# Optimization experiments

Measured on AMD Instinct MI355X. Metric: run time of the kernel, lower is better.

Reference implementation:

```python
import jax, jax.numpy as jnp
import numpy as np

# Dims (match init_kwargs / input_specs)
B, N, DIM, HEADS, DHEAD, CHUNK = 1, 2048, 1024, 8, 128, 64
HID = 4 * DHEAD            # MemoryMLP expansion_factor=4.0
DI = HEADS * DHEAD         # dim_inner
EPS = 1e-6
MAX_LR = 1.0               # default_step_transform_max_lr


def rmsnorm(x, w):
    return x * jax.lax.rsqrt(jnp.mean(jnp.square(x), -1, keepdims=True) + EPS) * w


def mem_forward(w0, w1, g, x):
    # ResidualNorm(MemoryMLP): y = RMSNorm(gelu(x@w0)@w1)*g + x
    h = jax.nn.gelu(x @ w0, approximate=False) @ w1
    return rmsnorm(h, g) + x


def setup_inputs() -> dict:
    key = jax.random.key(0)
    ks = jax.random.split(key, 12)
    s = lambda i, shape, sc: jax.random.normal(ks[i], shape, jnp.float32) * sc
    return dict(
        x=s(0, (B, N, DIM), 1.0),
        store_norm_w=jnp.ones((DIM,), jnp.float32),
        ret_norm_w=jnp.ones((DIM,), jnp.float32),
        Wq=s(1, (DIM, DI), DIM ** -0.5),
        Wk=s(2, (DIM, DI), DIM ** -0.5),
        Wv=s(3, (DIM, DI), DIM ** -0.5),
        W_step=s(4, (DIM, HEADS), DIM ** -0.5), b_step=jnp.zeros((HEADS,), jnp.float32),
        W_mom=s(5, (DIM, HEADS), DIM ** -0.5), b_mom=jnp.zeros((HEADS,), jnp.float32),
        W_decay=s(6, (DIM, HEADS), DIM ** -0.5), b_decay=jnp.zeros((HEADS,), jnp.float32),
        gate_W=s(7, (DIM, HEADS), DIM ** -0.5),
        combine_W=s(8, (DI, DIM), DI ** -0.5),
        mem_w0=s(9, (HEADS, DHEAD, HID), DHEAD ** -0.5),
        mem_w1=s(10, (HEADS, HID, DHEAD), HID ** -0.5),
        mem_g=jnp.ones((HEADS, DHEAD), jnp.float32),
    )


def reference(x, store_norm_w, ret_norm_w, Wq, Wk, Wv, W_step, b_step,
              W_mom, b_mom, W_decay, b_decay, gate_W, combine_W,
              mem_w0, mem_w1, mem_g):
    b, n, _ = x.shape
    nc = n // CHUNK
    BH = b * HEADS

    # ---- store path ----
    s = rmsnorm(x, store_norm_w)                                 # b n dim
    lr = jax.nn.sigmoid(s @ W_step + b_step) * MAX_LR            # b n h (per-token adaptive step)
    pooled = s.reshape(b, nc, CHUNK, DIM).mean(2)                # b nc dim (AveragePool chunk rep)
    mom = jax.nn.sigmoid(pooled @ W_mom + b_mom)                 # b nc h
    dec = jax.nn.sigmoid(pooled @ W_decay + b_decay)             # b nc h

    def to_chunks(t):  # b n (h d) -> (b h) nc c d
        return t.reshape(b, nc, CHUNK, HEADS, DHEAD).transpose(0, 3, 1, 2, 4).reshape(BH, nc, CHUNK, DHEAD)

    k = to_chunks(s @ Wk)
    v = to_chunks(s @ Wv)
    lr_c = lr.reshape(b, nc, CHUNK, HEADS).transpose(0, 3, 1, 2).reshape(BH, nc, CHUNK)
    mom_bh = mom.transpose(0, 2, 1).reshape(BH, nc)
    dec_bh = dec.transpose(0, 2, 1).reshape(BH, nc)

    # init fast weights per (b h)  (per_head_learned_parameters=True)
    w0 = jnp.broadcast_to(mem_w0[None], (b, HEADS, DHEAD, HID)).reshape(BH, DHEAD, HID)
    w1 = jnp.broadcast_to(mem_w1[None], (b, HEADS, HID, DHEAD)).reshape(BH, HID, DHEAD)
    g = jnp.broadcast_to(mem_g[None], (b, HEADS, DHEAD)).reshape(BH, DHEAD)

    def chunk_loss(w0_, w1_, g_, kc, vc, lrc):
        pred = mem_forward(w0_, w1_, g_, kc)                     # c d
        return jnp.sum(jnp.mean(jnp.square(pred - vc), -1) * lrc)

    grad_chunk = jax.grad(chunk_loss, argnums=(0, 1, 2))
    # vmap over chunks (same weights per chunk, per-sample grads), then over (b h)
    grads = jax.vmap(jax.vmap(grad_chunk, in_axes=(None, None, None, 0, 0, 0)))(w0, w1, g, k, v, lr_c)
    surprises = tuple(-gr for gr in grads)                       # each (BH, nc, ...)

    def combine(a, c):
        ga, xa = a
        gb, xb = c
        return (ga * gb, gb * xa + xb)

    def lin_scan(gates, xs):
        # y_i = gates_i * y_{i-1} + xs_i over chunk axis (axis=1)
        return jax.lax.associative_scan(combine, (gates, xs), axis=1)

    def expand(gates, ref):
        return gates.reshape(gates.shape + (1,) * (ref.ndim - 2))

    # momentum scan per parameter tensor
    updates = tuple(lin_scan(expand(mom_bh, su), su)[1] for su in surprises)

    # weight update scan: W_i = (1 - decay_i) * W_{i-1} + momentum_i, W_{-1} = init
    per_chunk_weights = []
    for upd, w_init in zip(updates, (w0, w1, g)):
        gates = expand(1.0 - dec_bh, upd)
        cumg, y = lin_scan(gates, upd)
        w_seq = y + cumg * w_init[:, None]                       # (BH, nc, ...)
        # retrieval at chunk i uses weights updated through chunk i-1
        per_chunk_weights.append(jnp.concatenate([w_init[:, None], w_seq[:, :-1]], axis=1))
    w0_c, w1_c, g_c = per_chunk_weights

    # ---- retrieve path ----
    r = rmsnorm(x, ret_norm_w)
    q = to_chunks(r @ Wq)                                        # (BH, nc, c, d)
    pred = jax.vmap(jax.vmap(mem_forward))(w0_c, w1_c, g_c, q)   # (BH, nc, c, d)
    out = pred.reshape(b, HEADS, n, DHEAD)                       # b h n d
    gate = jax.nn.sigmoid(r @ gate_W)                            # b n h (retrieve_gate, heads>1)
    out = out * gate.transpose(0, 2, 1)[..., None]
    out = out.transpose(0, 2, 1, 3).reshape(b, n, DI) @ combine_W
    return out
```

## Files before the change

### kernel.cpp

```cpp
#include <hip/hip_runtime.h>
#include <hip/hip_bf16.h>
#include <math.h>

#define NH   8
#define DHD  128
#define HIDN 512
#define CHK  64
#define NCH  32
#define MB   1048576ull

typedef unsigned short u16;
typedef unsigned int   u32;
typedef short s16x8 __attribute__((ext_vector_type(8)));
typedef float f32x4 __attribute__((ext_vector_type(4)));

#define MFMA(a,b,c) __builtin_amdgcn_mfma_f32_16x16x32_bf16((a),(b),(c),0,0,0)

__device__ __forceinline__ float bf2f(u16 v){ return __uint_as_float(((u32)v) << 16); }
__device__ __forceinline__ u16 f2bf(float f){
  u32 u = __float_as_uint(f);
  u += 0x7fffu + ((u >> 16) & 1u);
  return (u16)(u >> 16);
}
__device__ __forceinline__ u32 pack2(float a, float b){
  return (u32)f2bf(a) | ((u32)f2bf(b) << 16);
}
__device__ __forceinline__ float dot2(u32 a, u32 b){
  return __uint_as_float(a << 16)*__uint_as_float(b << 16)
       + __uint_as_float(a & 0xffff0000u)*__uint_as_float(b & 0xffff0000u);
}
__device__ __forceinline__ float waveRedSum(float v){
  #pragma unroll
  for (int off = 32; off; off >>= 1) v += __shfl_xor(v, off);
  return v;
}
__device__ __forceinline__ void gload16(const void* g, void* l){
  __builtin_amdgcn_global_load_lds(
      (const __attribute__((address_space(1))) u32*)g,
      (__attribute__((address_space(3))) u32*)l, 16, 0, 0);
}
__device__ __forceinline__ int swzb(int row, int colb){ return colb ^ ((row & 7) << 4); }
__device__ __forceinline__ int swza(int row, int colb){
  return colb ^ ((row & 7) << 4) ^ (((row >> 3) & 3) << 5);
}


__global__ __launch_bounds__(256) void k_prep(
    const float* __restrict__ Wq, const float* __restrict__ Wk,
    const float* __restrict__ Wv, const float* __restrict__ combW,
    const float* __restrict__ mw0, const float* __restrict__ mw1,
    const float* __restrict__ Wstep, const float* __restrict__ gateW,
    u16* __restrict__ WqT, u16* __restrict__ WkT, u16* __restrict__ WvT, u16* __restrict__ combT,
    u16* __restrict__ w0L, u16* __restrict__ w1L, u16* __restrict__ w1bL, u16* __restrict__ WsgL){
  __shared__ u16 tile[32][34];
  int bid = blockIdx.x, t = threadIdx.x;
  if (bid < 4096){
    int z = bid >> 10, rem = bid & 1023;
    const float* in = (z==0)?Wq:(z==1)?Wk:(z==2)?Wv:combW;
    u16* out = (z==0)?WqT:(z==1)?WkT:(z==2)?WvT:combT;
    int c0 = (rem & 31)*32, r0 = (rem >> 5)*32;
    int tx = t & 31, ty = t >> 5;
    #pragma unroll
    for (int k = 0; k < 4; ++k) tile[ty+k*8][tx] = f2bf(in[(size_t)(r0+ty+k*8)*1024 + c0+tx]);
    __syncthreads();
    #pragma unroll
    for (int k = 0; k < 4; ++k) out[(size_t)(c0+ty+k*8)*1024 + r0+tx] = tile[tx][ty+k*8];
  } else if (bid < 10240){
    int b2 = bid - 4096;
    int which = b2 >> 11;
    int h = (b2 >> 8) & 7;
    int i = (b2 & 255)*256 + t;
    int r = i & 511, blk = i >> 9;
    int lg = r >> 7, lr = (r >> 3) & 15, e = r & 7;
    float v; u16* dst;
    if (which == 0){ int n0 = blk >> 2, ks = blk & 3; int hid = n0*16+lr, d = ks*32+lg*8+e;
      v = mw0[(size_t)h*65536 + (size_t)d*512 + hid]; dst = w0L; }
    else if (which == 1){ int n0 = blk >> 4, ks = blk & 15; int d = n0*16+lr, hid = ks*32+lg*8+e;
      v = mw1[(size_t)h*65536 + (size_t)hid*128 + d]; dst = w1L; }
    else { int n0 = blk >> 2, ks = blk & 3; int hid = n0*16+lr, d = ks*32+lg*8+e;
      v = mw1[(size_t)h*65536 + (size_t)hid*128 + d]; dst = w1bL; }
    dst[(size_t)h*65536 + i] = f2bf(v);
  } else {
    int i = (bid - 10240)*256 + t;
    if (i < 16384){
      int o = i >> 10, k = i & 1023;
      float v = (o < 8) ? Wstep[(size_t)k*8 + o] : gateW[(size_t)k*8 + (o-8)];
      WsgL[i] = f2bf(v);
    }
  }
}

__global__ __launch_bounds__(256) void k_rmsnorm(const float* __restrict__ x,
    const float* __restrict__ wst, const float* __restrict__ wrt,
    u16* __restrict__ s_bf, u16* __restrict__ r_bf){
  int row = blockIdx.x, t = threadIdx.x;
  float4 v = ((const float4*)(x + (size_t)row*1024))[t];
  float ss = v.x*v.x + v.y*v.y + v.z*v.z + v.w*v.w;
  ss = waveRedSum(ss);
  __shared__ float red[4];
  int wv = t >> 6, ln = t & 63;
  if (ln == 0) red[wv] = ss;
  __syncthreads();
  float rr = rsqrtf((red[0]+red[1]+red[2]+red[3])*(1.f/1024.f) + 1e-6f);
  float4 a = ((const float4*)wst)[t];
  float4 b = ((const float4*)wrt)[t];
  uint2 so = make_uint2(pack2(v.x*rr*a.x, v.y*rr*a.y), pack2(v.z*rr*a.z, v.w*rr*a.w));
  uint2 ro = make_uint2(pack2(v.x*rr*b.x, v.y*rr*b.y), pack2(v.z*rr*b.z, v.w*rr*b.w));
  *(uint2*)(s_bf + (size_t)row*1024 + t*4) = so;
  *(uint2*)(r_bf + (size_t)row*1024 + t*4) = ro;
}

__global__ __launch_bounds__(256) void k_lrmd(const u16* __restrict__ s_bf, const u16* __restrict__ r_bf,
    const u16* __restrict__ WsgL, const float* __restrict__ bstep,
    const float* __restrict__ Wmom, const float* __restrict__ bmom,
    const float* __restrict__ Wdec, const float* __restrict__ bdec,
    float* __restrict__ lrc, float* __restrict__ gate,
    float* __restrict__ momb, float* __restrict__ decb){
  int bx = blockIdx.x;
  if (bx < 512){
    int wv = threadIdx.x >> 6, ln = threadIdx.x & 63;
    int tok = bx*4 + wv;
    const u16* sp = s_bf + (size_t)tok*1024 + ln*16;
    const u16* rp = r_bf + (size_t)tok*1024 + ln*16;
    uint4 s0 = *(const uint4*)sp, s1 = *(const uint4*)(sp+8);
    uint4 r0 = *(const uint4*)rp, r1 = *(const uint4*)(rp+8);
    #pragma unroll 4
    for (int o = 0; o < 16; ++o){
      const u16* wp = WsgL + (size_t)o*1024 + ln*16;
      uint4 w0v = *(const uint4*)wp, w1v = *(const uint4*)(wp+8);
      uint4 a0 = (o < 8) ? s0 : r0, a1 = (o < 8) ? s1 : r1;
      float acc = dot2(a0.x,w0v.x)+dot2(a0.y,w0v.y)+dot2(a0.z,w0v.z)+dot2(a0.w,w0v.w)
                + dot2(a1.x,w1v.x)+dot2(a1.y,w1v.y)+dot2(a1.z,w1v.z)+dot2(a1.w,w1v.w);
      acc = waveRedSum(acc);
      if (ln == 0){
        int h = o & 7;
        if (o < 8){
          float v = 1.f/(1.f+expf(-(acc + bstep[h])));
          lrc[((size_t)h*NCH + (tok>>6))*CHK + (tok&63)] = v;
        } else {
          gate[(size_t)tok*8 + h] = 1.f/(1.f+expf(-acc));
        }
      }
    }
  } else {
    __shared__ float plds[1024];
    int c = bx - 512, t = threadIdx.x;
    #pragma unroll
    for (int q = 0; q < 4; ++q){
      int d = q*256 + t;
      float acc = 0.f;
      for (int tt = 0; tt < 64; ++tt) acc += bf2f(s_bf[((size_t)c*64+tt)*1024 + d]);
      plds[d] = acc * (1.f/64.f);
    }
    __syncthreads();
    if (t < 64){
      int ln = t;
      for (int o = 0; o < 16; ++o){
        int h = o & 7;
        const float* W = (o < 8) ? Wmom : Wdec;
        float acc = 0.f;
        for (int k = ln; k < 1024; k += 64) acc += plds[k]*W[(size_t)k*8+h];
        acc = waveRedSum(acc);
        if (ln == 0){
          float bb = (o < 8) ? bmom[h] : bdec[h];
          float v = 1.f/(1.f+expf(-(acc+bb)));
          if (o < 8) momb[h*NCH + c] = v; else decb[h*NCH + c] = v;
        }
      }
    }
  }
}

__device__ __forceinline__ void gemm_body(const u16* __restrict__ A, const u16* __restrict__ BT,
    void* __restrict__ Cp, int mode){
  __shared__ char As[8192];
  __shared__ char Bs[16384];
  int t = threadIdx.x, l = t & 63, w = t >> 6, lr16 = l & 15, lg = l >> 4;
  int wm = w & 1, wn = w >> 1;
  int bm = blockIdx.x*64, bn = blockIdx.y*128;
  f32x4 acc[2][2];
  #pragma unroll
  for (int mt = 0; mt < 2; ++mt)
    #pragma unroll
    for (int nt = 0; nt < 2; ++nt) acc[mt][nt] = (f32x4){0.f,0.f,0.f,0.f};
  for (int k0 = 0; k0 < 1024; k0 += 64){
    gload16(A  + (size_t)(bm + (t>>3))*1024      + k0 + (t&7)*8, As + w*1024);
    gload16(BT + (size_t)(bn + (t>>3))*1024      + k0 + (t&7)*8, Bs + w*1024);
    gload16(BT + (size_t)(bn + 64 + (t>>3))*1024 + k0 + (t&7)*8, Bs + 8192 + w*1024);
    __syncthreads();
    #pragma unroll
    for (int ks = 0; ks < 2; ++ks){
      s16x8 xa[2], yb[2];
      #pragma unroll
      for (int mt = 0; mt < 2; ++mt){ int row = wm*32 + mt*16 + lr16;
        xa[mt] = *(const s16x8*)(As + row*128 + ks*64 + lg*16); }
      #pragma unroll
      for (int nt = 0; nt < 2; ++nt){ int row = wn*32 + nt*16 + lr16;
        yb[nt] = *(const s16x8*)(Bs + row*128 + ks*64 + lg*16); }
      #pragma unroll
      for (int mt = 0; mt < 2; ++mt)
        #pragma unroll
        for (int nt = 0; nt < 2; ++nt) acc[mt][nt] = MFMA(xa[mt], yb[nt], acc[mt][nt]);
    }
    __syncthreads();
  }
  #pragma unroll
  for (int mt = 0; mt < 2; ++mt)
    #pragma unroll
    for (int nt = 0; nt < 2; ++nt)
      #pragma unroll
      for (int j = 0; j < 4; ++j){
        int row = bm + wm*32 + mt*16 + lg*4 + j;
        int coln = bn + wn*32 + nt*16 + lr16;
        if (mode == 0) ((float*)Cp)[(size_t)row*1024 + coln] = acc[mt][nt][j];
        else { int cI = row>>6, tok = row&63, h = coln>>7, d = coln&127;
          ((u16*)Cp)[((size_t)(h*32+cI)*64 + tok)*128 + d] = f2bf(acc[mt][nt][j]); }
      }
}

__global__ __launch_bounds__(512) void k_gemm_bf(const u16* __restrict__ A, const u16* __restrict__ BT,
    void* __restrict__ Cp, int mode){ gemm_body(A, BT, Cp, mode); }

__global__ __launch_bounds__(512) void k_gemm3(
    const u16* __restrict__ s_bf, const u16* __restrict__ r_bf,
    const u16* __restrict__ WkT, const u16* __restrict__ WvT, const u16* __restrict__ WqT,
    u16* __restrict__ Kc, u16* __restrict__ Vc, u16* __restrict__ Qc){
  int z = blockIdx.z;
  const u16* A = (z==2) ? r_bf : s_bf;
  const u16* BT = (z==0) ? WkT : (z==1) ? WvT : WqT;
  u16* C = (z==0) ? Kc : (z==1) ? Vc : Qc;
  gemm_body(A, BT, (void*)C, 1);
}

__global__ __launch_bounds__(512) void k_grad(
    const u16* __restrict__ Kc, const u16* __restrict__ Vc, const float* __restrict__ lrc,
    const u16* __restrict__ w0L, const u16* __restrict__ w1L, const u16* __restrict__ w1bL,
    const float* __restrict__ mg,
    u16* __restrict__ SW0, u16* __restrict__ SW1, float* __restrict__ SG){
  extern __shared__ char sm[];
  char* a_s   = sm;
  char* upT_s = sm + 65536;
  char* dh_s  = sm + 131072;
  char* dhT_s = sm + 147456;
  char* duT_s = a_s;
  char* kcT_s = upT_s;
  float* scr  = (float*)dh_s;

  int c = blockIdx.x, bh = blockIdx.y, t = threadIdx.x;
  size_t bc = (size_t)bh*NCH + c;
  int l = t & 63, w = t >> 6, lr16 = l & 15, lg = l >> 4;
  int tg = w & 3, dhf = w >> 2;
  int tokb = tg*16, tok0 = tokb + lg*4;

  const u16* kc_g = Kc + bc*8192;
  const u16* vc_g = Vc + bc*8192;

  s16x8 xk[4];
  #pragma unroll
  for (int k = 0; k < 4; ++k)
    xk[k] = *(const s16x8*)(kc_g + (size_t)(tokb+lr16)*128 + k*32 + lg*8);
  const u16* w0Lh = w0L + (size_t)bh*65536;
  for (int n0h = 0; n0h < 16; ++n0h){
    int n0 = dhf*16 + n0h;
    f32x4 acc = {0.f,0.f,0.f,0.f};
    const u16* yb = w0Lh + (size_t)n0*2048 + l*8;
    #pragma unroll
    for (int k = 0; k < 4; ++k) acc = MFMA(xk[k], *(const s16x8*)(yb + k*512), acc);
    int hid = n0*16 + lr16;
    float upv[4];
    #pragma unroll
    for (int j = 0; j < 4; ++j){
      int tok = tok0 + j;
      float u = acc[j];
      float cdf = 0.5f*(1.f + erff(u*0.70710678118654752f));
      upv[j] = cdf + u*0.3989422804014327f*expf(-0.5f*u*u);
      *(u16*)(a_s + tok*1024 + swza(tok, hid*2)) = f2bf(u*cdf);
    }
    *(uint2*)(upT_s + hid*128 + swzb(hid, tok0*2)) =
        make_uint2(pack2(upv[0], upv[1]), pack2(upv[2], upv[3]));
  }
  __syncthreads();

  s16x8 xa[16];
  #pragma unroll
  for (int k = 0; k < 16; ++k){ int row = tokb + lr16;
    xa[k] = *(const s16x8*)(a_s + row*1024 + swza(row, (k*32+lg*8)*2)); }
  const u16* w1Lh = w1L + (size_t)bh*65536;
  f32x4 hD[4];
  #pragma unroll
  for (int n0l = 0; n0l < 4; ++n0l){
    f32x4 acc = {0.f,0.f,0.f,0.f};
    const u16* yb = w1Lh + (size_t)(dhf*4 + n0l)*8192 + l*8;
    #pragma unroll
    for (int k = 0; k < 16; ++k) acc = MFMA(xa[k], *(const s16x8*)(yb + k*512), acc);
    hD[n0l] = acc;
  }
  #pragma unroll
  for (int j = 0; j < 4; ++j){
    float s = 0.f;
    #pragma unroll
    for (int n0l = 0; n0l < 4; ++n0l) s += hD[n0l][j]*hD[n0l][j];
    s += __shfl_xor(s,1); s += __shfl_xor(s,2); s += __shfl_xor(s,4); s += __shfl_xor(s,8);
    if (lr16 == 0) scr[dhf*64 + tok0 + j] = s;
  }
  __syncthreads();
  float rv[4], lrv[4], dotp[4];
  #pragma unroll
  for (int j = 0; j < 4; ++j){
    int tok = tok0 + j;
    float tot = scr[tok] + scr[64 + tok];
    rv[j] = rsqrtf(tot*(1.f/128.f) + 1e-6f);
    lrv[j] = lrc[bc*64 + tok];
    dotp[j] = 0.f;
  }
  float dn[4][4];
  #pragma unroll
  for (int n0l = 0; n0l < 4; ++n0l){
    int d = dhf*64 + n0l*16 + lr16;
    float g0 = mg[(size_t)bh*128 + d];
    float dgav = 0.f;
    #pragma unroll
    for (int j = 0; j < 4; ++j){
      int tok = tok0 + j;
      float h = hD[n0l][j];
      float nrm = h*rv[j];
      float kcv = bf2f(kc_g[(size_t)tok*128 + d]);
      float vcv = bf2f(vc_g[(size_t)tok*128 + d]);
      float p = nrm*g0 + kcv;
      float dp = (2.f/128.f)*lrv[j]*(p - vcv);
      dgav += dp*nrm;
      float dnv = dp*g0;
      dn[n0l][j] = dnv;
      dotp[j] += dnv*h;
    }
    dgav += __shfl_xor(dgav,16); dgav += __shfl_xor(dgav,32);
    if (lg == 0) scr[256 + w*64 + n0l*16 + lr16] = dgav;
  }
  #pragma unroll
  for (int j = 0; j < 4; ++j){
    float dd = dotp[j];
    dd += __shfl_xor(dd,1); dd += __shfl_xor(dd,2); dd += __shfl_xor(dd,4); dd += __shfl_xor(dd,8);
    if (lr16 == 0) scr[128 + dhf*64 + tok0 + j] = dd;
  }
  __syncthreads();
  float dotv[4];
  #pragma unroll
  for (int j = 0; j < 4; ++j){
    int tok = tok0 + j;
    dotv[j] = scr[128 + tok] + scr[128 + 64 + tok];
  }
  if (t < 128){
    int dh2 = t >> 6, dl = t & 63;
    float s = scr[256 + (dh2*4+0)*64 + dl] + scr[256 + (dh2*4+1)*64 + dl]
            + scr[256 + (dh2*4+2)*64 + dl] + scr[256 + (dh2*4+3)*64 + dl];
    SG[bc*128 + t] = -s;
  }
  __syncthreads();
  #pragma unroll
  for (int n0l = 0; n0l < 4; ++n0l){
    int d = dhf*64 + n0l*16 + lr16;
    float dhv[4];
    #pragma unroll
    for (int j = 0; j < 4; ++j){
      int tok = tok0 + j;
      float c3 = rv[j]*rv[j]*rv[j]*(1.f/128.f);
      dhv[j] = rv[j]*dn[n0l][j] - c3*dotv[j]*hD[n0l][j];
      *(u16*)(dh_s + tok*256 + swzb(tok, d*2)) = f2bf(dhv[j]);
    }
    *(uint2*)(dhT_s + d*128 + swzb(d, tok0*2)) =
        make_uint2(pack2(dhv[0], dhv[1]), pack2(dhv[2], dhv[3]));
  }
  __syncthreads();

  {
    s16x8 yB[4][2];
    #pragma unroll
    for (int n0l = 0; n0l < 4; ++n0l){
      int hid = w*64 + n0l*16 + lr16;
      #pragma unroll
      for (int ks = 0; ks < 2; ++ks){
        s16x8 v;
        #pragma unroll
        for (int e = 0; e < 8; ++e){ int tok = ks*32 + lg*8 + e;
          v[e] = *(const short*)(a_s + tok*1024 + swza(tok, hid*2)); }
        yB[n0l][ks] = v;
      }
    }
    __syncthreads();
    u16* stg = (u16*)(a_s + w*8192);
    #pragma unroll 1
    for (int half = 0; half < 2; ++half){
      #pragma unroll
      for (int mt4 = 0; mt4 < 4; ++mt4){
        int mt = half*4 + mt4; int row = mt*16 + lr16;
        s16x8 xD0 = *(const s16x8*)(dhT_s + row*128 + swzb(row, (lg*8)*2));
        s16x8 xD1 = *(const s16x8*)(dhT_s + row*128 + swzb(row, (32+lg*8)*2));
        #pragma unroll
        for (int n0l = 0; n0l < 4; ++n0l){
          f32x4 acc = {0.f,0.f,0.f,0.f};
          acc = MFMA(xD0, yB[n0l][0], acc);
          acc = MFMA(xD1, yB[n0l][1], acc);
          int base = mt4*1024 + (n0l>>1)*512 + (((n0l*2)+(lr16>>3))&3)*128 + (lr16&7);
          #pragma unroll
          for (int j = 0; j < 4; ++j)
            stg[base + (lg*4+j)*8] = f2bf(-acc[j]);
        }
      }
      asm volatile("s_waitcnt lgkmcnt(0)" ::: "memory");
      #pragma unroll
      for (int mt4 = 0; mt4 < 4; ++mt4){
        int mt = half*4 + mt4;
        u16* gb = SW1 + bc*65536 + (size_t)(mt*16 + w*2)*512;
        s16x8 o0 = *(const s16x8*)(stg + mt4*1024 + l*16);
        s16x8 o1 = *(const s16x8*)(stg + mt4*1024 + l*16 + 8);
        *(s16x8*)(gb + l*16) = o0;
        *(s16x8*)(gb + l*16 + 8) = o1;
      }
    }
  }
  __syncthreads();

  {
    s16x8 xDh[4][4];
    #pragma unroll
    for (int mt = 0; mt < 4; ++mt){ int row = mt*16 + lr16;
      #pragma unroll
      for (int ks = 0; ks < 4; ++ks)
        xDh[mt][ks] = *(const s16x8*)(dh_s + row*256 + swzb(row, (ks*32+lg*8)*2)); }
    const u16* w1bh = w1bL + (size_t)bh*65536;
    #pragma unroll 2
    for (int n0l = 0; n0l < 4; ++n0l){
      int hid = w*64 + n0l*16 + lr16;
      s16x8 yW[4];
      const u16* xb = w1bh + (size_t)(w*4 + n0l)*2048 + l*8;
      #pragma unroll
      for (int ks = 0; ks < 4; ++ks)
        yW[ks] = *(const s16x8*)(xb + ks*512);
      #pragma unroll
      for (int mt = 0; mt < 4; ++mt){
        f32x4 acc = {0.f,0.f,0.f,0.f};
        #pragma unroll
        for (int ks = 0; ks < 4; ++ks) acc = MFMA(xDh[mt][ks], yW[ks], acc);
        int tk0 = mt*16 + lg*4;
        uint2 ur = *(const uint2*)(upT_s + hid*128 + swzb(hid, tk0*2));
        float u0 = bf2f((u16)(ur.x & 0xffff)), u1 = bf2f((u16)(ur.x >> 16));
        float u2 = bf2f((u16)(ur.y & 0xffff)), u3 = bf2f((u16)(ur.y >> 16));
        *(uint2*)(duT_s + hid*128 + swzb(hid, tk0*2)) =
            make_uint2(pack2(acc[0]*u0, acc[1]*u1), pack2(acc[2]*u2, acc[3]*u3));
      }
    }
  }
  __syncthreads();

  #pragma unroll
  for (int i = 0; i < 2; ++i){
    int idx = i*512 + t;
    int tok = idx & 63, d0 = (idx >> 6)*8;
    s16x8 kv = *(const s16x8*)(kc_g + (size_t)tok*128 + d0);
    #pragma unroll
    for (int e = 0; e < 8; ++e)
      *(u16*)(kcT_s + (d0+e)*128 + swzb(d0+e, tok*2)) = kv[e];
  }
  __syncthreads();

  {
    s16x8 yK[8][2];
    #pragma unroll
    for (int n0 = 0; n0 < 8; ++n0){
      int d = n0*16 + lr16;
      #pragma unroll
      for (int ks = 0; ks < 2; ++ks)
        yK[n0][ks] = *(const s16x8*)(kcT_s + d*128 + swzb(d, (ks*32+lg*8)*2));
    }
    #pragma unroll 1
    for (int mi = 0; mi < 4; ++mi){
      int hid = w*64 + mi*16 + lr16;
      s16x8 xU0 = *(const s16x8*)(duT_s + hid*128 + swzb(hid, (lg*8)*2));
      s16x8 xU1 = *(const s16x8*)(duT_s + hid*128 + swzb(hid, (32+lg*8)*2));
      u16* stgw = (u16*)(duT_s + (size_t)(w*64 + mi*16)*128);
      u16* gb = SW0 + bc*65536 + (size_t)(w*4 + mi)*2048;
      #pragma unroll 1
      for (int hh = 0; hh < 2; ++hh){
        #pragma unroll
        for (int n0h = 0; n0h < 4; ++n0h){
          int n0 = hh*4 + n0h;
          f32x4 acc = {0.f,0.f,0.f,0.f};
          acc = MFMA(xU0, yK[n0][0], acc);
          acc = MFMA(xU1, yK[n0][1], acc);
          int base = (n0h>>1)*512 + (((n0h*2)+(lr16>>3))&3)*128 + (lr16&7);
          #pragma unroll
          for (int j = 0; j < 4; ++j)
            stgw[base + (lg*4+j)*8] = f2bf(-acc[j]);
        }
        asm volatile("s_waitcnt lgkmcnt(0)" ::: "memory");
        s16x8 o0 = *(const s16x8*)(stgw + l*16);
        s16x8 o1 = *(const s16x8*)(stgw + l*16 + 8);
        *(s16x8*)(gb + hh*1024 + l*16) = o0;
        *(s16x8*)(gb + hh*1024 + l*16 + 8) = o1;
      }
    }
  }
}

__global__ __launch_bounds__(256) void k_scan(
    const u16* __restrict__ w0L, const u16* __restrict__ w1L, const float* __restrict__ mg,
    const u16* __restrict__ SW0, const u16* __restrict__ SW1, const float* __restrict__ SG,
    const float* __restrict__ momb, const float* __restrict__ decb,
    u16* __restrict__ W0C, u16* __restrict__ W1C, float* __restrict__ GC){
  int bh = blockIdx.y, bx = blockIdx.x, t = threadIdx.x;
  const float* momp = momb + bh*NCH;
  const float* decp = decb + bh*NCH;
  if (bx < 64){
    int which = bx >> 5;
    int e0 = ((bx & 31)*256 + t)*8;
    const u16* wL = which ? w1L : w0L;
    const u16* SW = which ? SW1 : SW0;
    u16* WC = which ? W1C : W0C;
    float Wv[8], m[8];
    uint4 wv = *(const uint4*)(wL + (size_t)bh*65536 + e0);
    const u16* wp = (const u16*)&wv;
    #pragma unroll
    for (int q = 0; q < 8; ++q){ Wv[q] = bf2f(wp[q]); m[q] = 0.f; }
    const u16* su = SW + (size_t)bh*NCH*65536 + e0;
    u16* outp = WC + (size_t)bh*NCH*65536 + e0;
    for (int cc = 0; cc < NCH; ++cc){
      uint4 ov;
      u16* op = (u16*)&ov;
      #pragma unroll
      for (int q = 0; q < 8; ++q) op[q] = f2bf(Wv[q]);
      *(uint4*)(outp + (size_t)cc*65536) = ov;
      uint4 sv = *(const uint4*)(su + (size_t)cc*65536);
      const u16* sp2 = (const u16*)&sv;
      float mo = momp[cc], de = 1.f - decp[cc];
      #pragma unroll
      for (int q = 0; q < 8; ++q){
        m[q] = mo*m[q] + bf2f(sp2[q]);
        Wv[q] = de*Wv[q] + m[q];
      }
    }
  } else {
    if (t >= 128) return;
    float Wv = mg[(size_t)bh*128 + t], m = 0.f;
    const float* su = SG + (size_t)bh*NCH*128 + t;
    float* outp = GC + (size_t)bh*NCH*128 + t;
    for (int cc = 0; cc < NCH; ++cc){
      outp[(size_t)cc*128] = Wv;
      m = momp[cc]*m + su[(size_t)cc*128];
      Wv = (1.f - decp[cc])*Wv + m;
    }
  }
}

__global__ __launch_bounds__(512) void k_retr(
    const u16* __restrict__ Qc, const u16* __restrict__ W0C, const u16* __restrict__ W1C,
    const float* __restrict__ GC, const float* __restrict__ gate, u16* __restrict__ OH){
  extern __shared__ char sm[];
  char* a_s = sm;
  float* scr = (float*)(sm + 65536);
  int c = blockIdx.x, bh = blockIdx.y, t = threadIdx.x;
  size_t bc = (size_t)bh*NCH + c;
  int l = t & 63, w = t >> 6, lr16 = l & 15, lg = l >> 4;
  int tg = w & 3, dhf = w >> 2;
  const u16* q_g = Qc + bc*8192;

  s16x8 xq[4];
  #pragma unroll
  for (int k = 0; k < 4; ++k)
    xq[k] = *(const s16x8*)(q_g + (size_t)(tg*16+lr16)*128 + k*32 + lg*8);
  const u16* w0c = W0C + bc*65536;
  for (int n0h = 0; n0h < 16; ++n0h){
    int n0 = dhf*16 + n0h;
    f32x4 acc = {0.f,0.f,0.f,0.f};
    const u16* yb = w0c + (size_t)n0*2048 + l*8;
    #pragma unroll
    for (int k = 0; k < 4; ++k) acc = MFMA(xq[k], *(const s16x8*)(yb + k*512), acc);
    int hid = n0*16 + lr16;
    #pragma unroll
    for (int j = 0; j < 4; ++j){
      int tok = tg*16 + lg*4 + j;
      float u = acc[j];
      float av = u*0.5f*(1.f + erff(u*0.70710678118654752f));
      *(u16*)(a_s + tok*1024 + swza(tok, hid*2)) = f2bf(av);
    }
  }
  __syncthreads();
  s16x8 xa[16];
  #pragma unroll
  for (int k = 0; k < 16; ++k){ int row = tg*16 + lr16;
    xa[k] = *(const s16x8*)(a_s + row*1024 + swza(row, (k*32+lg*8)*2)); }
  const u16* w1c = W1C + bc*65536;
  f32x4 hD[4];
  #pragma unroll
  for (int n0l = 0; n0l < 4; ++n0l){
    f32x4 acc = {0.f,0.f,0.f,0.f};
    const u16* yb = w1c + (size_t)(dhf*4 + n0l)*8192 + l*8;
    #pragma unroll
    for (int k = 0; k < 16; ++k) acc = MFMA(xa[k], *(const s16x8*)(yb + k*512), acc);
    hD[n0l] = acc;
  }
  #pragma unroll
  for (int j = 0; j < 4; ++j){
    float s = 0.f;
    #pragma unroll
    for (int n0l = 0; n0l < 4; ++n0l) s += hD[n0l][j]*hD[n0l][j];
    s += __shfl_xor(s,1); s += __shfl_xor(s,2); s += __shfl_xor(s,4); s += __shfl_xor(s,8);
    if (lr16 == 0) scr[dhf*64 + tg*16 + lg*4 + j] = s;
  }
  __syncthreads();
  float rv[4], gtv[4];
  #pragma unroll
  for (int j = 0; j < 4; ++j){
    int tok = tg*16 + lg*4 + j;
    rv[j] = rsqrtf((scr[tok] + scr[64 + tok])*(1.f/128.f) + 1e-6f);
    gtv[j] = gate[(size_t)(c*64 + tok)*8 + bh];
  }
  #pragma unroll
  for (int n0l = 0; n0l < 4; ++n0l){
    int d = dhf*64 + n0l*16 + lr16;
    float g0 = GC[bc*128 + d];
    #pragma unroll
    for (int j = 0; j < 4; ++j){
      int tok = tg*16 + lg*4 + j; int tokg = c*64 + tok;
      float qv = bf2f(q_g[(size_t)tok*128 + d]);
      float p = hD[n0l][j]*rv[j]*g0 + qv;
      OH[(size_t)tokg*1024 + bh*128 + d] = f2bf(p*gtv[j]);
    }
  }
}

extern "C" void kernel_launch(void* const* d_in, const int* in_sizes, int n_in,
                              void* d_out, int out_size, void* d_ws, size_t ws_size,
                              hipStream_t stream) {
  (void)in_sizes; (void)n_in; (void)out_size; (void)ws_size;
  const float* x     = (const float*)d_in[0];
  const float* snw   = (const float*)d_in[1];
  const float* rnw   = (const float*)d_in[2];
  const float* Wq    = (const float*)d_in[3];
  const float* Wk    = (const float*)d_in[4];
  const float* Wv    = (const float*)d_in[5];
  const float* Wstep = (const float*)d_in[6];
  const float* bstep = (const float*)d_in[7];
  const float* Wmom  = (const float*)d_in[8];
  const float* bmom  = (const float*)d_in[9];
  const float* Wdec  = (const float*)d_in[10];
  const float* bdec  = (const float*)d_in[11];
  const float* gateW = (const float*)d_in[12];
  const float* combW = (const float*)d_in[13];
  const float* mw0   = (const float*)d_in[14];
  const float* mw1   = (const float*)d_in[15];
  const float* mg    = (const float*)d_in[16];
  float* out = (float*)d_out;

  char* Wb = (char*)d_ws;
  u16* Qc    = (u16*)(Wb + 0*MB);
  u16* Kc    = (u16*)(Wb + 4*MB);
  u16* Vc    = (u16*)(Wb + 8*MB);
  u16* s_bf  = (u16*)(Wb + 12*MB);
  u16* r_bf  = (u16*)(Wb + 16*MB);
  u16* WqT   = (u16*)(Wb + 20*MB);
  u16* WkT   = (u16*)(Wb + 22*MB);
  u16* WvT   = (u16*)(Wb + 24*MB);
  u16* combT = (u16*)(Wb + 26*MB);
  u16* w0L   = (u16*)(Wb + 28*MB);
  u16* w1L   = (u16*)(Wb + 29*MB);
  u16* w1bL  = (u16*)(Wb + 30*MB);
  u16* OH    = (u16*)(Wb + 31*MB);
  u16* SW0   = (u16*)(Wb + 35*MB);
  u16* SW1   = (u16*)(Wb + 67*MB);
  u16* W0C   = (u16*)(Wb + 99*MB);
  u16* W1C   = (u16*)(Wb + 131*MB);
  float* lrc    = (float*)(Wb + 163*MB + 131072);
  float* momb   = (float*)(Wb + 163*MB + 196608);
  float* decb   = (float*)(Wb + 163*MB + 197632);
  float* gate   = (float*)(Wb + 163*MB + 198656);
  float* SG     = (float*)(Wb + 163*MB + 264192);
  float* GC     = (float*)(Wb + 163*MB + 395264);
  u16* WsgL  = (u16*)(Wb + 163*MB + 526336);

  hipFuncSetAttribute((const void*)k_grad, hipFuncAttributeMaxDynamicSharedMemorySize, 163840);
  hipFuncSetAttribute((const void*)k_retr, hipFuncAttributeMaxDynamicSharedMemorySize, 66560);

  k_prep<<<10304, 256, 0, stream>>>(Wq, Wk, Wv, combW, mw0, mw1, Wstep, gateW,
                                    WqT, WkT, WvT, combT, w0L, w1L, w1bL, WsgL);
  k_rmsnorm<<<2048, 256, 0, stream>>>(x, snw, rnw, s_bf, r_bf);
  k_lrmd<<<544, 256, 0, stream>>>(s_bf, r_bf, WsgL, bstep, Wmom, bmom, Wdec, bdec,
                                  lrc, gate, momb, decb);
  k_gemm3<<<dim3(32,8,3), 512, 0, stream>>>(s_bf, r_bf, WkT, WvT, WqT, Kc, Vc, Qc);
  k_grad<<<dim3(32,8), 512, 163840, stream>>>(Kc, Vc, lrc, w0L, w1L, w1bL, mg, SW0, SW1, SG);
  k_scan<<<dim3(65,8), 256, 0, stream>>>(w0L, w1L, mg, SW0, SW1, SG, momb, decb, W0C, W1C, GC);
  k_retr<<<dim3(32,8), 512, 66560, stream>>>(Qc, W0C, W1C, GC, gate, OH);
  k_gemm_bf<<<dim3(32,8), 512, 0, stream>>>(OH, combT, (void*)out, 0);
}
```

Before: 233.6 us.

## Split monolithic gradient kernel into four smaller stage kernels with global intermediates

Replaces the single large-LDS k_grad kernel (163 KB shared, one block per chunk-head) with four kernels. kG1 computes the first MLP layer with GELU, kG2 computes the second layer as a tiled GEMM using a newly transposed w1, kE1 handles the RMSNorm backward and loss gradient, and kB forms the weight-gradient products. The aim is more blocks, lower LDS use per block and therefore better occupancy. The cost is extra launches and global round-trips for the a, up, h and dh intermediates, which live in scratch regions reused from later buffers.

```diff
diff --git a/kernel.cpp b/kernel.cpp
--- a/kernel.cpp
+++ b/kernel.cpp
@@ -51,7 +51,8 @@
     const float* __restrict__ mw0, const float* __restrict__ mw1,
     const float* __restrict__ Wstep, const float* __restrict__ gateW,
     u16* __restrict__ WqT, u16* __restrict__ WkT, u16* __restrict__ WvT, u16* __restrict__ combT,
-    u16* __restrict__ w0L, u16* __restrict__ w1L, u16* __restrict__ w1bL, u16* __restrict__ WsgL){
+    u16* __restrict__ w0L, u16* __restrict__ w1L, u16* __restrict__ w1bL, u16* __restrict__ WsgL,
+    u16* __restrict__ w1T){
   __shared__ u16 tile[32][34];
   int bid = blockIdx.x, t = threadIdx.x;
   if (bid < 4096){
@@ -80,13 +81,25 @@
     else { int n0 = blk >> 2, ks = blk & 3; int hid = n0*16+lr, d = ks*32+lg*8+e;
       v = mw1[(size_t)h*65536 + (size_t)hid*128 + d]; dst = w1bL; }
     dst[(size_t)h*65536 + i] = f2bf(v);
-  } else {
+  } else if (bid < 10304){
     int i = (bid - 10240)*256 + t;
     if (i < 16384){
       int o = i >> 10, k = i & 1023;
       float v = (o < 8) ? Wstep[(size_t)k*8 + o] : gateW[(size_t)k*8 + (o-8)];
       WsgL[i] = f2bf(v);
     }
+  } else {
+    int b3 = bid - 10304;
+    int h = b3 >> 6, ti = b3 & 63;
+    int c0 = (ti & 3)*32, r0 = (ti >> 2)*32;
+    int tx = t & 31, ty = t >> 5;
+    #pragma unroll
+    for (int k = 0; k < 4; ++k)
+      tile[ty+k*8][tx] = f2bf(mw1[(size_t)h*65536 + (size_t)(r0+ty+k*8)*128 + c0+tx]);
+    __syncthreads();
+    #pragma unroll
+    for (int k = 0; k < 4; ++k)
+      w1T[(size_t)h*65536 + (size_t)(c0+ty+k*8)*512 + r0+tx] = tile[tx][ty+k*8];
   }
 }
 
@@ -232,143 +245,196 @@
   gemm_body(A, BT, (void*)C, 1);
 }
 
-__global__ __launch_bounds__(512) void k_grad(
-    const u16* __restrict__ Kc, const u16* __restrict__ Vc, const float* __restrict__ lrc,
-    const u16* __restrict__ w0L, const u16* __restrict__ w1L, const u16* __restrict__ w1bL,
-    const float* __restrict__ mg,
-    u16* __restrict__ SW0, u16* __restrict__ SW1, float* __restrict__ SG){
+__global__ __launch_bounds__(512) void kG1(
+    const u16* __restrict__ Kc, const u16* __restrict__ w0L,
+    u16* __restrict__ a_g, u16* __restrict__ up_g){
+  __shared__ char As[16384];
+  __shared__ u16 stg[2][8192];
+  int t = threadIdx.x, l = t & 63, w = t >> 6, lr16 = l & 15, lg = l >> 4;
+  int bm = blockIdx.x*64, hb = blockIdx.y*128, h = blockIdx.z;
+  const u16* A = Kc + (size_t)h*262144;
+  #pragma unroll
+  for (int i = 0; i < 2; ++i){
+    int idx = i*512 + t;
+    int row = idx >> 4, seg = idx & 15;
+    int segp = seg ^ (row & 7);
+    gload16(A + (size_t)(bm+row)*128 + segp*8, As + i*8192 + w*1024);
+  }
+  __syncthreads();
+  int n0 = (hb >> 4) + w;
+  const u16* yb = w0L + (size_t)h*65536 + (size_t)n0*2048 + l*8;
+  s16x8 yf[4];
+  #pragma unroll
+  for (int ks = 0; ks < 4; ++ks) yf[ks] = *(const s16x8*)(yb + ks*512);
+  int hidL = w*16 + lr16;
+  #pragma unroll
+  for (int mt = 0; mt < 4; ++mt){
+    s16x8 xa[4];
+    #pragma unroll
+    for (int ks = 0; ks < 4; ++ks){ int row = mt*16 + lr16;
+      xa[ks] = *(const s16x8*)(As + row*256 + swzb(row, (ks*32+lg*8)*2)); }
+    f32x4 acc = {0.f,0.f,0.f,0.f};
+    #pragma unroll
+    for (int ks = 0; ks < 4; ++ks) acc = MFMA(xa[ks], yf[ks], acc);
+    #pragma unroll
+    for (int j = 0; j < 4; ++j){
+      int tok = mt*16 + lg*4 + j;
+      float u = acc[j];
+      float cdf = 0.5f*(1.f + erff(u*0.70710678118654752f));
+      float upv = cdf + u*0.3989422804014327f*expf(-0.5f*u*u);
+      stg[0][tok*128 + hidL] = f2bf(u*cdf);
+      stg[1][tok*128 + hidL] = f2bf(upv);
+    }
+  }
+  __syncthreads();
+  #pragma unroll
+  for (int i = 0; i < 4; ++i){
+    int idx = i*512 + t;
+    int arr = idx >> 10;
+    int e = (idx & 1023)*8;
+    int tok = e >> 7, colL = e & 127;
+    s16x8 v = *(const s16x8*)(&stg[arr][tok*128 + colL]);
+    u16* dst = (arr ? up_g : a_g) + (size_t)h*1048576 + (size_t)(bm+tok)*512 + hb + colL;
+    *(s16x8*)dst = v;
+  }
+}
+
+__global__ __launch_bounds__(512) void kG2(
+    const u16* __restrict__ a_g, const u16* __restrict__ w1T, float* __restrict__ h_g){
+  __shared__ char As[8192];
+  __shared__ char Bs[16384];
+  int t = threadIdx.x, l = t & 63, w = t >> 6, lr16 = l & 15, lg = l >> 4;
+  int wm = w & 1, wn = w >> 1;
+  int bm = blockIdx.x*64, h = blockIdx.y;
+  const u16* A = a_g + (size_t)h*1048576;
+  const u16* BT = w1T + (size_t)h*65536;
+  f32x4 acc[2][2];
+  #pragma unroll
+  for (int mt = 0; mt < 2; ++mt)
+    #pragma unroll
+    for (int nt = 0; nt < 2; ++nt) acc[mt][nt] = (f32x4){0.f,0.f,0.f,0.f};
+  for (int k0 = 0; k0 < 512; k0 += 64){
+    gload16(A  + (size_t)(bm + (t>>3))*512 + k0 + (t&7)*8, As + w*1024);
+    gload16(BT + (size_t)(t>>3)*512        + k0 + (t&7)*8, Bs + w*1024);
+    gload16(BT + (size_t)(64 + (t>>3))*512 + k0 + (t&7)*8, Bs + 8192 + w*1024);
+    __syncthreads();
+    #pragma unroll
+    for (int ks = 0; ks < 2; ++ks){
+      s16x8 xa[2], yb[2];
+      #pragma unroll
+      for (int mt = 0; mt < 2; ++mt){ int row = wm*32 + mt*16 + lr16;
+        xa[mt] = *(const s16x8*)(As + row*128 + ks*64 + lg*16); }
+      #pragma unroll
+      for (int nt = 0; nt < 2; ++nt){ int row = wn*32 + nt*16 + lr16;
+        yb[nt] = *(const s16x8*)(Bs + row*128 + ks*64 + lg*16); }
+      #pragma unroll
+      for (int mt = 0; mt < 2; ++mt)
+        #pragma unroll
+        for (int nt = 0; nt < 2; ++nt) acc[mt][nt] = MFMA(xa[mt], yb[nt], acc[mt][nt]);
+    }
+    __syncthreads();
+  }
+  float* C = h_g + (size_t)h*262144;
+  #pragma unroll
+  for (int mt = 0; mt < 2; ++mt)
+    #pragma unroll
+    for (int nt = 0; nt < 2; ++nt)
+      #pragma unroll
+      for (int j = 0; j < 4; ++j){
+        int row = bm + wm*32 + mt*16 + lg*4 + j;
+        int coln = wn*32 + nt*16 + lr16;
+        C[(size_t)row*128 + coln] = acc[mt][nt][j];
+      }
+}
+
+__global__ __launch_bounds__(256) void kE1(
+    const float* __restrict__ h_g, const u16* __restrict__ Kc, const u16* __restrict__ Vc,
+    const float* __restrict__ lrc, const float* __restrict__ mg,
+    u16* __restrict__ dh_g, float* __restrict__ SG){
+  __shared__ float sgl[512];
+  int c = blockIdx.x, h = blockIdx.y, t = threadIdx.x;
+  size_t bc = (size_t)h*NCH + c;
+  int l = t & 63, w = t >> 6;
+  int tok = t >> 2, q = t & 3, d0 = q*32;
+  const float* hr = h_g + (size_t)h*262144 + (size_t)(c*64+tok)*128 + d0;
+  float hv[32];
+  #pragma unroll
+  for (int i = 0; i < 32; i += 4) *(float4*)&hv[i] = *(const float4*)(hr + i);
+  float ss = 0.f;
+  #pragma unroll
+  for (int i = 0; i < 32; ++i) ss += hv[i]*hv[i];
+  ss += __shfl_xor(ss,1); ss += __shfl_xor(ss,2);
+  float rv = rsqrtf(ss*(1.f/128.f) + 1e-6f);
+  float lr = lrc[bc*64 + tok];
+  s16x8 kvv[4], vvv[4];
+  const u16* kp = Kc + bc*8192 + (size_t)tok*128 + d0;
+  const u16* vp = Vc + bc*8192 + (size_t)tok*128 + d0;
+  #pragma unroll
+  for (int b = 0; b < 4; ++b){ kvv[b] = *(const s16x8*)(kp + b*8); vvv[b] = *(const s16x8*)(vp + b*8); }
+  const float* mgp = mg + (size_t)h*128 + d0;
+  float dg[32], dn[32], dot = 0.f;
+  const u16* kr = (const u16*)kvv; const u16* vr = (const u16*)vvv;
+  #pragma unroll
+  for (int i = 0; i < 32; ++i){
+    float g0 = mgp[i];
+    float nrm = hv[i]*rv;
+    float p = nrm*g0 + bf2f(kr[i]);
+    float dp = (2.f/128.f)*lr*(p - bf2f(vr[i]));
+    dg[i] = dp*nrm;
+    float d = dp*g0;
+    dn[i] = d;
+    dot += d*hv[i];
+  }
+  dot += __shfl_xor(dot,1); dot += __shfl_xor(dot,2);
+  float c3 = rv*rv*rv*(1.f/128.f);
+  u16 ob[32];
+  #pragma unroll
+  for (int i = 0; i < 32; ++i) ob[i] = f2bf(rv*dn[i] - c3*dot*hv[i]);
+  u16* dpo = dh_g + (size_t)h*262144 + (size_t)(c*64+tok)*128 + d0;
+  #pragma unroll
+  for (int b = 0; b < 4; ++b) *(s16x8*)(dpo + b*8) = *(const s16x8*)&ob[b*8];
+  #pragma unroll
+  for (int off = 4; off <= 32; off <<= 1){
+    #pragma unroll
+    for (int i = 0; i < 32; ++i) dg[i] += __shfl_xor(dg[i], off);
+  }
+  if ((l >> 2) == 0){
+    #pragma unroll
+    for (int i = 0; i < 32; ++i) sgl[w*128 + l*32 + i] = dg[i];
+  }
+  __syncthreads();
+  if (t < 128) SG[bc*128 + t] = -(sgl[t] + sgl[128+t] + sgl[256+t] + sgl[384+t]);
+}
+
+__global__ __launch_bounds__(512) void kB(
+    const u16* __restrict__ Kc, const u16* __restrict__ a_g, const u16* __restrict__ up_g,
+    const u16* __restrict__ dh_g, const u16* __restrict__ w1bL,
+    u16* __restrict__ SW0, u16* __restrict__ SW1){
   extern __shared__ char sm[];
   char* a_s   = sm;
-  char* upT_s = sm + 65536;
-  char* dh_s  = sm + 131072;
-  char* dhT_s = sm + 147456;
+  char* dhT_s = sm + 65536;
   char* duT_s = a_s;
-  char* kcT_s = upT_s;
-  float* scr  = (float*)dh_s;
-
-  int c = blockIdx.x, bh = blockIdx.y, t = threadIdx.x;
-  size_t bc = (size_t)bh*NCH + c;
+  char* kcT_s = dhT_s;
+  int c = blockIdx.x, h = blockIdx.y, t = threadIdx.x;
+  size_t bc = (size_t)h*NCH + c;
   int l = t & 63, w = t >> 6, lr16 = l & 15, lg = l >> 4;
-  int tg = w & 3, dhf = w >> 2;
-  int tokb = tg*16, tok0 = tokb + lg*4;
-
-  const u16* kc_g = Kc + bc*8192;
-  const u16* vc_g = Vc + bc*8192;
-
-  s16x8 xk[4];
-  #pragma unroll
-  for (int k = 0; k < 4; ++k)
-    xk[k] = *(const s16x8*)(kc_g + (size_t)(tokb+lr16)*128 + k*32 + lg*8);
-  const u16* w0Lh = w0L + (size_t)bh*65536;
-  for (int n0h = 0; n0h < 16; ++n0h){
-    int n0 = dhf*16 + n0h;
-    f32x4 acc = {0.f,0.f,0.f,0.f};
-    const u16* yb = w0Lh + (size_t)n0*2048 + l*8;
-    #pragma unroll
-    for (int k = 0; k < 4; ++k) acc = MFMA(xk[k], *(const s16x8*)(yb + k*512), acc);
-    int hid = n0*16 + lr16;
-    float upv[4];
-    #pragma unroll
-    for (int j = 0; j < 4; ++j){
-      int tok = tok0 + j;
-      float u = acc[j];
-      float cdf = 0.5f*(1.f + erff(u*0.70710678118654752f));
-      upv[j] = cdf + u*0.3989422804014327f*expf(-0.5f*u*u);
-      *(u16*)(a_s + tok*1024 + swza(tok, hid*2)) = f2bf(u*cdf);
-    }
-    *(uint2*)(upT_s + hid*128 + swzb(hid, tok0*2)) =
-        make_uint2(pack2(upv[0], upv[1]), pack2(upv[2], upv[3]));
-  }
-  __syncthreads();
-
-  s16x8 xa[16];
-  #pragma unroll
-  for (int k = 0; k < 16; ++k){ int row = tokb + lr16;
-    xa[k] = *(const s16x8*)(a_s + row*1024 + swza(row, (k*32+lg*8)*2)); }
-  const u16* w1Lh = w1L + (size_t)bh*65536;
-  f32x4 hD[4];
-  #pragma unroll
-  for (int n0l = 0; n0l < 4; ++n0l){
-    f32x4 acc = {0.f,0.f,0.f,0.f};
-    const u16* yb = w1Lh + (size_t)(dhf*4 + n0l)*8192 + l*8;
-    #pragma unroll
-    for (int k = 0; k < 16; ++k) acc = MFMA(xa[k], *(const s16x8*)(yb + k*512), acc);
-    hD[n0l] = acc;
-  }
-  #pragma unroll
-  for (int j = 0; j < 4; ++j){
-    float s = 0.f;
-    #pragma unroll
-    for (int n0l = 0; n0l < 4; ++n0l) s += hD[n0l][j]*hD[n0l][j];
-    s += __shfl_xor(s,1); s += __shfl_xor(s,2); s += __shfl_xor(s,4); s += __shfl_xor(s,8);
-    if (lr16 == 0) scr[dhf*64 + tok0 + j] = s;
-  }
-  __syncthreads();
-  float rv[4], lrv[4], dotp[4];
-  #pragma unroll
-  for (int j = 0; j < 4; ++j){
-    int tok = tok0 + j;
-    float tot = scr[tok] + scr[64 + tok];
-    rv[j] = rsqrtf(tot*(1.f/128.f) + 1e-6f);
-    lrv[j] = lrc[bc*64 + tok];
-    dotp[j] = 0.f;
-  }
-  float dn[4][4];
-  #pragma unroll
-  for (int n0l = 0; n0l < 4; ++n0l){
-    int d = dhf*64 + n0l*16 + lr16;
-    float g0 = mg[(size_t)bh*128 + d];
-    float dgav = 0.f;
-    #pragma unroll
-    for (int j = 0; j < 4; ++j){
-      int tok = tok0 + j;
-      float h = hD[n0l][j];
-      float nrm = h*rv[j];
-      float kcv = bf2f(kc_g[(size_t)tok*128 + d]);
-      float vcv = bf2f(vc_g[(size_t)tok*128 + d]);
-      float p = nrm*g0 + kcv;
-      float dp = (2.f/128.f)*lrv[j]*(p - vcv);
-      dgav += dp*nrm;
-      float dnv = dp*g0;
-      dn[n0l][j] = dnv;
-      dotp[j] += dnv*h;
-    }
-    dgav += __shfl_xor(dgav,16); dgav += __shfl_xor(dgav,32);
-    if (lg == 0) scr[256 + w*64 + n0l*16 + lr16] = dgav;
-  }
-  #pragma unroll
-  for (int j = 0; j < 4; ++j){
-    float dd = dotp[j];
-    dd += __shfl_xor(dd,1); dd += __shfl_xor(dd,2); dd += __shfl_xor(dd,4); dd += __shfl_xor(dd,8);
-    if (lr16 == 0) scr[128 + dhf*64 + tok0 + j] = dd;
-  }
-  __syncthreads();
-  float dotv[4];
-  #pragma unroll
-  for (int j = 0; j < 4; ++j){
-    int tok = tok0 + j;
-    dotv[j] = scr[128 + tok] + scr[128 + 64 + tok];
-  }
-  if (t < 128){
-    int dh2 = t >> 6, dl = t & 63;
-    float s = scr[256 + (dh2*4+0)*64 + dl] + scr[256 + (dh2*4+1)*64 + dl]
-            + scr[256 + (dh2*4+2)*64 + dl] + scr[256 + (dh2*4+3)*64 + dl];
-    SG[bc*128 + t] = -s;
-  }
-  __syncthreads();
-  #pragma unroll
-  for (int n0l = 0; n0l < 4; ++n0l){
-    int d = dhf*64 + n0l*16 + lr16;
-    float dhv[4];
-    #pragma unroll
-    for (int j = 0; j < 4; ++j){
-      int tok = tok0 + j;
-      float c3 = rv[j]*rv[j]*rv[j]*(1.f/128.f);
-      dhv[j] = rv[j]*dn[n0l][j] - c3*dotv[j]*hD[n0l][j];
-      *(u16*)(dh_s + tok*256 + swzb(tok, d*2)) = f2bf(dhv[j]);
-    }
-    *(uint2*)(dhT_s + d*128 + swzb(d, tok0*2)) =
-        make_uint2(pack2(dhv[0], dhv[1]), pack2(dhv[2], dhv[3]));
+  const u16* dh_b = dh_g + (size_t)h*262144 + (size_t)c*64*128;
+
+  #pragma unroll
+  for (int i = 0; i < 8; ++i){
+    int idx = i*512 + t;
+    int tok = idx >> 6, seg = idx & 63;
+    s16x8 v = *(const s16x8*)(a_g + (size_t)h*1048576 + (size_t)(c*64+tok)*512 + seg*8);
+    *(s16x8*)(a_s + tok*1024 + swza(tok, seg*16)) = v;
+  }
+  #pragma unroll
+  for (int i = 0; i < 2; ++i){
+    int idx = i*512 + t;
+    int tok = idx & 63, d0 = (idx >> 6)*8;
+    s16x8 v = *(const s16x8*)(dh_b + (size_t)tok*128 + d0);
+    #pragma unroll
+    for (int e = 0; e < 8; ++e)
+      *(u16*)(dhT_s + (d0+e)*128 + swzb(d0+e, tok*2)) = v[e];
   }
   __syncthreads();
 
@@ -423,11 +489,12 @@
   {
     s16x8 xDh[4][4];
     #pragma unroll
-    for (int mt = 0; mt < 4; ++mt){ int row = mt*16 + lr16;
+    for (int mt = 0; mt < 4; ++mt){
       #pragma unroll
       for (int ks = 0; ks < 4; ++ks)
-        xDh[mt][ks] = *(const s16x8*)(dh_s + row*256 + swzb(row, (ks*32+lg*8)*2)); }
-    const u16* w1bh = w1bL + (size_t)bh*65536;
+        xDh[mt][ks] = *(const s16x8*)(dh_b + (size_t)(mt*16+lr16)*128 + ks*32 + lg*8);
+    }
+    const u16* w1bh = w1bL + (size_t)h*65536;
     #pragma unroll 2
     for (int n0l = 0; n0l < 4; ++n0l){
       int hid = w*64 + n0l*16 + lr16;
@@ -442,9 +509,8 @@
         #pragma unroll
         for (int ks = 0; ks < 4; ++ks) acc = MFMA(xDh[mt][ks], yW[ks], acc);
         int tk0 = mt*16 + lg*4;
-        uint2 ur = *(const uint2*)(upT_s + hid*128 + swzb(hid, tk0*2));
-        float u0 = bf2f((u16)(ur.x & 0xffff)), u1 = bf2f((u16)(ur.x >> 16));
-        float u2 = bf2f((u16)(ur.y & 0xffff)), u3 = bf2f((u16)(ur.y >> 16));
+        const u16* ub = up_g + (size_t)h*1048576 + (size_t)(c*64+tk0)*512 + hid;
+        float u0 = bf2f(ub[0]), u1 = bf2f(ub[512]), u2 = bf2f(ub[1024]), u3 = bf2f(ub[1536]);
         *(uint2*)(duT_s + hid*128 + swzb(hid, tk0*2)) =
             make_uint2(pack2(acc[0]*u0, acc[1]*u1), pack2(acc[2]*u2, acc[3]*u3));
       }
@@ -456,7 +522,7 @@
   for (int i = 0; i < 2; ++i){
     int idx = i*512 + t;
     int tok = idx & 63, d0 = (idx >> 6)*8;
-    s16x8 kv = *(const s16x8*)(kc_g + (size_t)tok*128 + d0);
+    s16x8 kv = *(const s16x8*)(Kc + bc*8192 + (size_t)tok*128 + d0);
     #pragma unroll
     for (int e = 0; e < 8; ++e)
       *(u16*)(kcT_s + (d0+e)*128 + swzb(d0+e, tok*2)) = kv[e];
@@ -669,6 +735,10 @@
   u16* SW1   = (u16*)(Wb + 67*MB);
   u16* W0C   = (u16*)(Wb + 99*MB);
   u16* W1C   = (u16*)(Wb + 131*MB);
+  float* h_g = (float*)(Wb + 35*MB);
+  u16* a_g   = (u16*)(Wb + 99*MB);
+  u16* up_g  = (u16*)(Wb + 115*MB);
+  u16* dh_g  = (u16*)(Wb + 131*MB);
   float* lrc    = (float*)(Wb + 163*MB + 131072);
   float* momb   = (float*)(Wb + 163*MB + 196608);
   float* decb   = (float*)(Wb + 163*MB + 197632);
@@ -676,17 +746,21 @@
   float* SG     = (float*)(Wb + 163*MB + 264192);
   float* GC     = (float*)(Wb + 163*MB + 395264);
   u16* WsgL  = (u16*)(Wb + 163*MB + 526336);
-
-  hipFuncSetAttribute((const void*)k_grad, hipFuncAttributeMaxDynamicSharedMemorySize, 163840);
+  u16* w1T   = (u16*)(Wb + 164*MB);
+
+  hipFuncSetAttribute((const void*)kB,     hipFuncAttributeMaxDynamicSharedMemorySize, 81920);
   hipFuncSetAttribute((const void*)k_retr, hipFuncAttributeMaxDynamicSharedMemorySize, 66560);
 
-  k_prep<<<10304, 256, 0, stream>>>(Wq, Wk, Wv, combW, mw0, mw1, Wstep, gateW,
-                                    WqT, WkT, WvT, combT, w0L, w1L, w1bL, WsgL);
+  k_prep<<<10816, 256, 0, stream>>>(Wq, Wk, Wv, combW, mw0, mw1, Wstep, gateW,
+                                    WqT, WkT, WvT, combT, w0L, w1L, w1bL, WsgL, w1T);
   k_rmsnorm<<<2048, 256, 0, stream>>>(x, snw, rnw, s_bf, r_bf);
   k_lrmd<<<544, 256, 0, stream>>>(s_bf, r_bf, WsgL, bstep, Wmom, bmom, Wdec, bdec,
                                   lrc, gate, momb, decb);
   k_gemm3<<<dim3(32,8,3), 512, 0, stream>>>(s_bf, r_bf, WkT, WvT, WqT, Kc, Vc, Qc);
-  k_grad<<<dim3(32,8), 512, 163840, stream>>>(Kc, Vc, lrc, w0L, w1L, w1bL, mg, SW0, SW1, SG);
+  kG1<<<dim3(32,4,8), 512, 0, stream>>>(Kc, w0L, a_g, up_g);
+  kG2<<<dim3(32,8), 512, 0, stream>>>(a_g, w1T, h_g);
+  kE1<<<dim3(32,8), 256, 0, stream>>>(h_g, Kc, Vc, lrc, mg, dh_g, SG);
+  kB<<<dim3(32,8), 512, 81920, stream>>>(Kc, a_g, up_g, dh_g, w1bL, SW0, SW1);
   k_scan<<<dim3(65,8), 256, 0, stream>>>(w0L, w1L, mg, SW0, SW1, SG, momb, decb, W0C, W1C, GC);
   k_retr<<<dim3(32,8), 512, 66560, stream>>>(Qc, W0C, W1C, GC, gate, OH);
   k_gemm_bf<<<dim3(32,8), 512, 0, stream>>>(OH, combT, (void*)out, 0);
```

Measured after the change: 254.5 us. +8.9%, slower.
